# Performance work log

Measured on AMD Instinct MI355X. Metric: run time of the kernel, lower is better.

Reference implementation:

```python
import jax, jax.numpy as jnp
import numpy as np

EPS = 1e-5
KH = KW = 3  # deformable kernel
K = KH * KW


def _offset_conv(w, woff, boff):
    # standard 3x3 conv, stride 1, padding 1, NCHW
    out = jax.lax.conv_general_dilated(
        w, woff, window_strides=(1, 1), padding='SAME',
        dimension_numbers=('NCHW', 'OIHW', 'NCHW'))
    return out + boff[None, :, None, None]


def _deform_conv(feat, offset, wd, bd):
    # feat: [B,C,H,W]; offset: [B,2K,H,W] with (dy,dx) pairs per kernel point
    B, C, H, W = feat.shape
    off = offset.reshape(B, K, 2, H, W)
    ii = jnp.arange(H, dtype=feat.dtype)[:, None]  # [H,1]
    jj = jnp.arange(W, dtype=feat.dtype)[None, :]  # [1,W]
    kk = jnp.arange(K)
    ky = (kk // KW - 1).astype(feat.dtype)[None, :, None, None]  # [1,K,1,1]
    kx = (kk % KW - 1).astype(feat.dtype)[None, :, None, None]
    py = ii[None, None] + ky + off[:, :, 0]  # [B,K,H,W] sample rows
    px = jj[None, None] + kx + off[:, :, 1]  # [B,K,H,W] sample cols

    featf = feat.reshape(B, C, H * W)
    y0 = jnp.floor(py)
    x0 = jnp.floor(px)
    sampled = jnp.zeros((B, C, K, H, W), dtype=feat.dtype)
    for dy in (0, 1):
        for dx in (0, 1):
            yc = y0 + dy
            xc = x0 + dx
            wgt = (1.0 - jnp.abs(py - yc)) * (1.0 - jnp.abs(px - xc))
            valid = (yc >= 0) & (yc <= H - 1) & (xc >= 0) & (xc <= W - 1)
            wgt = jnp.where(valid, wgt, 0.0)  # zero padding outside
            yi = jnp.clip(yc, 0, H - 1).astype(jnp.int32)
            xi = jnp.clip(xc, 0, W - 1).astype(jnp.int32)
            idx = (yi * W + xi).reshape(B, 1, K * H * W)
            vals = jnp.take_along_axis(featf, idx, axis=2).reshape(B, C, K, H, W)
            sampled = sampled + vals * wgt[:, None]
    # weighted 3x3 conv over sampled points
    out = jnp.einsum('bckhw,ock->bohw', sampled, wd.reshape(wd.shape[0], C, K))
    return out + bd[None, :, None, None]


def setup_inputs() -> dict:
    key = jax.random.key(0)
    ks = jax.random.split(key, 13)
    B, Cin, H, W = 8, 256, 96, 96
    Cm = 64
    s1 = 1.0 / np.sqrt(Cin)
    s3 = 1.0 / np.sqrt(Cm * 9)
    return {
        'x': jax.random.normal(ks[0], (B, Cin, H, W), jnp.float32),
        'w1': jax.random.normal(ks[1], (Cm, Cin), jnp.float32) * s1,
        'b1': jax.random.normal(ks[2], (Cm,), jnp.float32) * s1,
        'woff': jax.random.normal(ks[3], (18, Cm, 3, 3), jnp.float32) * s3,
        'boff': jax.random.normal(ks[4], (18,), jnp.float32) * s3,
        'wd': jax.random.normal(ks[5], (Cm, Cm, 3, 3), jnp.float32) * s3,
        'bd': jax.random.normal(ks[6], (Cm,), jnp.float32) * s3,
        'gamma': jnp.ones((Cm,), jnp.float32),
        'beta': jnp.zeros((Cm,), jnp.float32),
        'rmean': jnp.zeros((Cm,), jnp.float32),
        'rvar': jax.random.uniform(ks[7], (Cm,), jnp.float32, 0.5, 1.5),
        'w2': jax.random.normal(ks[8], (Cin, Cm), jnp.float32) / np.sqrt(Cm),
        'b2': jax.random.normal(ks[9], (Cin,), jnp.float32) / np.sqrt(Cm),
    }


def reference(x, w1, b1, woff, boff, wd, bd, gamma, beta, rmean, rvar, w2, b2):
    # pwconv1 (1x1)
    w = jnp.einsum('bchw,oc->bohw', x, w1) + b1[None, :, None, None]
    # deformable 3x3 conv with predicted offsets
    off = _offset_conv(w, woff, boff)
    w = _deform_conv(w, off, wd, bd)
    # BatchNorm (eval mode, running stats)
    inv = gamma / jnp.sqrt(rvar + EPS)
    w = w * inv[None, :, None, None] + (beta - rmean * inv)[None, :, None, None]
    # pwconv2 (1x1) + sigmoid gate
    w = jnp.einsum('bchw,oc->bohw', w, w2) + b2[None, :, None, None]
    return x * jax.nn.sigmoid(w)
```

## Files before the change

kernel.cpp:

```cpp
#include <hip/hip_runtime.h>
#include <math.h>

#define H 96
#define W 96
#define HW 9216
#define B 8
#define CIN 256
#define CM 64
#define NPOS (B*HW)
#define NBLK (NPOS/64)

__device__ __forceinline__ int xswiz(int n) { return (n & 7) * 144 + (n >> 3); }

typedef float  f32x4  __attribute__((ext_vector_type(4)));
typedef short  bf16x8 __attribute__((ext_vector_type(8)));

#define OFF_WOFFT 0
#define OFF_BNS   10368
#define OFF_BNB   10432
#define OFF_WDB1  10496
#define OFF_WDB3  18688
#define OFF_WDB2  37120
#define OFF_FEAT  45312
#define OFF_FCL   4763904
#define OFF_OFFS  9482496
#define OFF_VCL   OFF_FEAT

__device__ __forceinline__ unsigned bfbits(float f) {
  union { float f; unsigned u; } c;
  c.f = f;
  return (c.u + 0x7FFFu + ((c.u >> 16) & 1u)) >> 16;
}
__device__ __forceinline__ short f2bf(float f) { return (short)bfbits(f); }
__device__ __forceinline__ unsigned pack2(float lo, float hi) {
  return bfbits(lo) | (bfbits(hi) << 16);
}

__device__ __forceinline__ bf16x8 cvt_frag(const float* p) {
  const float2* q = (const float2*)p;
  float2 a0 = q[0], a1 = q[1], a2 = q[2], a3 = q[3];
  union { unsigned u[4]; bf16x8 v; } r;
  r.u[0] = pack2(a0.x, a0.y);
  r.u[1] = pack2(a1.x, a1.y);
  r.u[2] = pack2(a2.x, a2.y);
  r.u[3] = pack2(a3.x, a3.y);
  return r.v;
}

__global__ __launch_bounds__(256) void k0_prep(
    const float* __restrict__ w1, const float* __restrict__ woff,
    const float* __restrict__ wd, const float* __restrict__ w2,
    const float* __restrict__ gamma, const float* __restrict__ beta,
    const float* __restrict__ rmean, const float* __restrict__ rvar,
    float* __restrict__ ws) {
  int i = blockIdx.x * 256 + threadIdx.x;
  if (i < 10368) {
    int c = i / 162, r = i - c * 162;
    int o = r / 9, k = r - o * 9;
    ws[OFF_WOFFT + i] = woff[(o * 64 + c) * 9 + k];
  } else if (i < 10432) {
    int o = i - 10368;
    float inv = gamma[o] / sqrtf(rvar[o] + 1e-5f);
    ws[OFF_BNS + o] = inv;
    ws[OFF_BNB + o] = beta[o] - rmean[o] * inv;
  } else if (i < 26816) {
    int j = i - 10432;
    int j8 = j & 7, lane = (j >> 3) & 63, nt = (j >> 9) & 3, kc = j >> 11;
    int n = nt * 16 + (lane & 15);
    int c = kc * 32 + ((lane >> 4) & 3) * 8 + j8;
    ((short*)(ws + OFF_WDB1))[j] = f2bf(w1[n * 256 + c]);
  } else if (i < 63680) {
    int j = i - 26816;
    int j8 = j & 7, lane = (j >> 3) & 63, nt = (j >> 9) & 3, kc = j >> 11;
    int n = nt * 16 + (lane & 15);
    int c = (kc & 1) * 32 + ((lane >> 4) & 3) * 8 + j8;
    int ks = kc >> 1;
    ((short*)(ws + OFF_WDB3))[j] = f2bf(wd[(n * 64 + c) * 9 + ks]);
  } else if (i < 80064) {
    int j = i - 63680;
    int j8 = j & 7, lane = (j >> 3) & 63, nt = (j >> 9) & 15, kc = j >> 13;
    int n = nt * 16 + (lane & 15);
    int c = kc * 32 + ((lane >> 4) & 3) * 8 + j8;
    ((short*)(ws + OFF_WDB2))[j] = f2bf(w2[n * 64 + c]);
  }
}

__global__ __launch_bounds__(256) void k1_pw1(
    const float* __restrict__ x, const short* __restrict__ wdb1,
    const float* __restrict__ b1, float* __restrict__ feat,
    float* __restrict__ fcl) {
  __shared__ float sA[64 * 66];
  int t = threadIdx.x;
  int lane = t & 63;
  int qq = __builtin_amdgcn_readfirstlane(t >> 6);
  int quad = lane >> 4, l15 = lane & 15;
  int mrow = qq * 16 + l15;
  int gpos0 = blockIdx.x * 64;
  int b = gpos0 / HW, hw0 = gpos0 - b * HW;
  f32x4 acc[4];
#pragma unroll
  for (int nt = 0; nt < 4; nt++) acc[nt] = (f32x4){0.f, 0.f, 0.f, 0.f};

  for (int c0 = 0; c0 < CIN; c0 += 64) {
#pragma unroll 4
    for (int it = 0; it < 16; it++) {
      int ci = it * 4 + quad;
      int p = qq * 16 + l15;
      sA[p * 66 + ci] = x[(size_t)(b * CIN + c0 + ci) * HW + hw0 + p];
    }
#pragma unroll
    for (int ch = 0; ch < 2; ch++) {
      bf16x8 af = cvt_frag(&sA[mrow * 66 + ch * 32 + quad * 8]);
      int kc = (c0 >> 5) + ch;
#pragma unroll
      for (int nt = 0; nt < 4; nt++) {
        bf16x8 bf = ((const bf16x8*)wdb1)[(kc * 4 + nt) * 64 + lane];
        acc[nt] = __builtin_amdgcn_mfma_f32_16x16x32_bf16(af, bf, acc[nt], 0, 0, 0);
      }
    }
  }
  __syncthreads();
#pragma unroll
  for (int nt = 0; nt < 4; nt++) {
    int o = nt * 16 + l15;
#pragma unroll
    for (int reg = 0; reg < 4; reg++) {
      int m = qq * 16 + quad * 4 + reg;
      sA[m * 66 + o] = acc[nt][reg] + b1[o];
    }
  }
  __syncthreads();
  for (int rr = t; rr < 4096; rr += 256) {
    int o1 = rr >> 6, p1 = rr & 63;
    feat[(size_t)(b * CM + o1) * HW + hw0 + p1] = sA[p1 * 66 + o1];
    int p2 = rr >> 6, o2 = rr & 63;
    fcl[(size_t)(gpos0 + p2) * 64 + o2] = sA[p2 * 66 + o2];
  }
}

__global__ __launch_bounds__(256) void k2_off(
    const float* __restrict__ feat, const float* __restrict__ wofft,
    const float* __restrict__ boff, float* __restrict__ offs) {
  __shared__ float part[4 * 18 * 64];
  int t = threadIdx.x;
  int pos = t & 63;
  int gg = __builtin_amdgcn_readfirstlane(t >> 6);
  int gpos0 = xswiz(blockIdx.x) * 64;
  int b = gpos0 / HW, hw0 = gpos0 - b * HW;
  int hw = hw0 + pos;
  int i = hw / W, j = hw - i * W;
  int idx9[9];
  float m9[9];
#pragma unroll
  for (int kh = 0; kh < 3; kh++)
#pragma unroll
    for (int kw = 0; kw < 3; kw++) {
      int yy = i + kh - 1, xx = j + kw - 1;
      bool ok = (yy >= 0) && (yy < H) && (xx >= 0) && (xx < W);
      idx9[kh * 3 + kw] = ok ? yy * W + xx : 0;
      m9[kh * 3 + kw] = ok ? 1.f : 0.f;
    }
  const float* fb = feat + (size_t)b * CM * HW;
  float acc[18];
#pragma unroll
  for (int o = 0; o < 18; o++) acc[o] = 0.f;
  for (int cc = 0; cc < 16; cc++) {
    int c = gg * 16 + cc;
    const float* fc = fb + c * HW;
    float v[9];
#pragma unroll
    for (int k = 0; k < 9; k++) v[k] = fc[idx9[k]] * m9[k];
    const float* wr = wofft + c * 162;
#pragma unroll
    for (int o = 0; o < 18; o++)
#pragma unroll
      for (int k = 0; k < 9; k++)
        acc[o] += v[k] * wr[o * 9 + k];
  }
#pragma unroll
  for (int o = 0; o < 18; o++) part[(gg * 18 + o) * 64 + pos] = acc[o];
  __syncthreads();
  for (int r = t; r < 18 * 64; r += 256) {
    int o = r >> 6, p = r & 63;
    float s = part[o * 64 + p] + part[(18 + o) * 64 + p] +
              part[(36 + o) * 64 + p] + part[(54 + o) * 64 + p] + boff[o];
    offs[(size_t)b * 18 * HW + o * HW + hw0 + p] = s;
  }
}

__global__ __launch_bounds__(256) void k3_deform(
    const float* __restrict__ fcl, const float* __restrict__ offs,
    const short* __restrict__ wdb3, const float* __restrict__ bd,
    const float* __restrict__ bns, const float* __restrict__ bnb,
    short* __restrict__ vclb) {
  __shared__ __align__(16) short sAb[64 * 72];
  __shared__ int2 tiw[4][576];
  int t = threadIdx.x;
  int lane = t & 63;
  int qq = __builtin_amdgcn_readfirstlane(t >> 6);
  int quad = lane >> 4, l15 = lane & 15;
  int mrow = qq * 16 + l15;
  int gpos0 = xswiz(blockIdx.x) * 64;
  int b = gpos0 / HW, hw0 = gpos0 - b * HW;
  int hw = hw0 + lane;
  int i = hw / W, j = hw - i * W;
  const float* ob = offs + (size_t)b * 18 * HW + hw;

  for (int k = qq; k < 9; k += 4) {
    float dy = ob[(2 * k + 0) * HW];
    float dx = ob[(2 * k + 1) * HW];
    float py = (float)(i + k / 3 - 1) + dy;
    float px = (float)(j + k % 3 - 1) + dx;
    float y0f = floorf(py), x0f = floorf(px);
    int y0 = (int)y0f, x0 = (int)x0f;
    float fy = py - y0f, fx = px - x0f;
    float w00 = (1.f - fy) * (1.f - fx), w01 = (1.f - fy) * fx;
    float w10 = fy * (1.f - fx), w11 = fy * fx;
    bool vy0 = (y0 >= 0) && (y0 < H), vy1 = (y0 + 1 >= 0) && (y0 + 1 < H);
    bool vx0 = (x0 >= 0) && (x0 < W), vx1 = (x0 + 1 >= 0) && (x0 + 1 < W);
    if (!(vy0 && vx0)) w00 = 0.f;
    if (!(vy0 && vx1)) w01 = 0.f;
    if (!(vy1 && vx0)) w10 = 0.f;
    if (!(vy1 && vx1)) w11 = 0.f;
    int yi0 = min(max(y0, 0), H - 1), yi1 = min(max(y0 + 1, 0), H - 1);
    int xi0 = min(max(x0, 0), W - 1), xi1 = min(max(x0 + 1, 0), W - 1);
    int e = k * 64 + lane;
    tiw[0][e] = make_int2((yi0 * W + xi0) * 256, __float_as_int(w00));
    tiw[1][e] = make_int2((yi0 * W + xi1) * 256, __float_as_int(w01));
    tiw[2][e] = make_int2((yi1 * W + xi0) * 256, __float_as_int(w10));
    tiw[3][e] = make_int2((yi1 * W + xi1) * 256, __float_as_int(w11));
  }
  __syncthreads();

  const char* fbase = (const char*)fcl + (size_t)b * HW * 256;
  int c2 = lane & 31;
  int c28 = c2 * 8;
  int half = lane >> 5;

  f32x4 acc[4];
#pragma unroll
  for (int nt = 0; nt < 4; nt++) acc[nt] = (f32x4){0.f, 0.f, 0.f, 0.f};

  for (int ks = 0; ks < 9; ks++) {
#pragma unroll 4
    for (int pp = 0; pp < 8; pp++) {
      int pa = qq * 16 + pp * 2 + half;
      int e = ks * 64 + pa;
      int2 t0 = tiw[0][e], t1 = tiw[1][e], t2 = tiw[2][e], t3 = tiw[3][e];
      float2 v0 = *(const float2*)(fbase + (t0.x + c28));
      float2 v1 = *(const float2*)(fbase + (t1.x + c28));
      float2 v2 = *(const float2*)(fbase + (t2.x + c28));
      float2 v3 = *(const float2*)(fbase + (t3.x + c28));
      float w0 = __int_as_float(t0.y), w1 = __int_as_float(t1.y);
      float w2 = __int_as_float(t2.y), w3 = __int_as_float(t3.y);
      float slo = w0 * v0.x + w1 * v1.x + w2 * v2.x + w3 * v3.x;
      float shi = w0 * v0.y + w1 * v1.y + w2 * v2.y + w3 * v3.y;
      ((unsigned*)sAb)[pa * 36 + c2] = pack2(slo, shi);
    }
#pragma unroll
    for (int ch = 0; ch < 2; ch++) {
      bf16x8 af = *(const bf16x8*)(sAb + mrow * 72 + ch * 32 + quad * 8);
      int kc = ks * 2 + ch;
#pragma unroll
      for (int nt = 0; nt < 4; nt++) {
        bf16x8 bf = ((const bf16x8*)wdb3)[(kc * 4 + nt) * 64 + lane];
        acc[nt] = __builtin_amdgcn_mfma_f32_16x16x32_bf16(af, bf, acc[nt], 0, 0, 0);
      }
    }
  }
  __syncthreads();
#pragma unroll
  for (int nt = 0; nt < 4; nt++) {
    int o = nt * 16 + l15;
    float sc = bns[o], sb = bnb[o], bb = bd[o];
#pragma unroll
    for (int reg = 0; reg < 4; reg++) {
      int m = qq * 16 + quad * 4 + reg;
      sAb[m * 72 + o] = f2bf((acc[nt][reg] + bb) * sc + sb);
    }
  }
  __syncthreads();
  for (int rr = t; rr < 2048; rr += 256) {
    int p = rr >> 5, cc = rr & 31;
    ((unsigned*)vclb)[(size_t)(gpos0 + p) * 32 + cc] = ((unsigned*)sAb)[p * 36 + cc];
  }
}

__global__ __launch_bounds__(256) void k4_pw2(
    const float* __restrict__ x, const short* __restrict__ vclb,
    const short* __restrict__ wdb2, const float* __restrict__ b2,
    float* __restrict__ out) {
  __shared__ float sA[64 * 66];
  int t = threadIdx.x;
  int lane = t & 63;
  int qq = __builtin_amdgcn_readfirstlane(t >> 6);
  int quad = lane >> 4, l15 = lane & 15;
  int mrow = qq * 16 + l15;
  int gpos0 = blockIdx.x * 64;
  int b = gpos0 / HW, hw0 = gpos0 - b * HW;

  const bf16x8* ap = (const bf16x8*)(vclb + (size_t)(gpos0 + mrow) * 64);
  bf16x8 af0 = ap[quad];
  bf16x8 af1 = ap[4 + quad];

  f32x4 acc[16];
#pragma unroll
  for (int nt = 0; nt < 16; nt++) acc[nt] = (f32x4){0.f, 0.f, 0.f, 0.f};
#pragma unroll
  for (int nt = 0; nt < 16; nt++) {
    bf16x8 bf0 = ((const bf16x8*)wdb2)[(0 * 16 + nt) * 64 + lane];
    bf16x8 bf1 = ((const bf16x8*)wdb2)[(1 * 16 + nt) * 64 + lane];
    acc[nt] = __builtin_amdgcn_mfma_f32_16x16x32_bf16(af0, bf0, acc[nt], 0, 0, 0);
    acc[nt] = __builtin_amdgcn_mfma_f32_16x16x32_bf16(af1, bf1, acc[nt], 0, 0, 0);
  }
  for (int nc = 0; nc < 4; nc++) {
    __syncthreads();
#pragma unroll
    for (int nt2 = 0; nt2 < 4; nt2++) {
      int nt = nc * 4 + nt2;
      int o1 = nt2 * 16 + l15;
#pragma unroll
      for (int reg = 0; reg < 4; reg++) {
        int m = qq * 16 + quad * 4 + reg;
        sA[m * 66 + o1] = acc[nt][reg] + b2[nc * 64 + nt2 * 16 + l15];
      }
    }
    __syncthreads();
    for (int rr = t; rr < 4096; rr += 256) {
      int o1 = rr >> 6, p = rr & 63;
      int o = nc * 64 + o1;
      float wv = sA[p * 66 + o1];
      float sg = 1.f / (1.f + __expf(-wv));
      size_t gi = ((size_t)b * CIN + o) * HW + hw0 + p;
      out[gi] = x[gi] * sg;
    }
  }
}

extern "C" void kernel_launch(void* const* d_in, const int* in_sizes, int n_in,
                              void* d_out, int out_size, void* d_ws, size_t ws_size,
                              hipStream_t stream) {
  const float* x     = (const float*)d_in[0];
  const float* w1    = (const float*)d_in[1];
  const float* b1    = (const float*)d_in[2];
  const float* woff  = (const float*)d_in[3];
  const float* boff  = (const float*)d_in[4];
  const float* wd    = (const float*)d_in[5];
  const float* bd    = (const float*)d_in[6];
  const float* gamma = (const float*)d_in[7];
  const float* beta  = (const float*)d_in[8];
  const float* rmean = (const float*)d_in[9];
  const float* rvar  = (const float*)d_in[10];
  const float* w2    = (const float*)d_in[11];
  const float* b2    = (const float*)d_in[12];
  float* out = (float*)d_out;
  float* ws  = (float*)d_ws;

  dim3 blk(256);
  k0_prep<<<dim3(313), blk, 0, stream>>>(w1, woff, wd, w2, gamma, beta, rmean, rvar, ws);
  k1_pw1<<<dim3(NBLK), blk, 0, stream>>>(x, (const short*)(ws + OFF_WDB1), b1,
                                         ws + OFF_FEAT, ws + OFF_FCL);
  k2_off<<<dim3(NBLK), blk, 0, stream>>>(ws + OFF_FEAT, ws + OFF_WOFFT, boff, ws + OFF_OFFS);
  k3_deform<<<dim3(NBLK), blk, 0, stream>>>(ws + OFF_FCL, ws + OFF_OFFS,
                                            (const short*)(ws + OFF_WDB3), bd,
                                            ws + OFF_BNS, ws + OFF_BNB,
                                            (short*)(ws + OFF_VCL));
  k4_pw2<<<dim3(NBLK), blk, 0, stream>>>(x, (const short*)(ws + OFF_VCL),
                                         (const short*)(ws + OFF_WDB2), b2, out);
}
```

Measured before the change: 302.6 us.

## Move offset conv to MFMA, drop NCHW feat copy, gather bilinear directly into fragments

The offset-prediction 3x3 conv now runs as a bf16 MFMA GEMM over the channels-last feature buffer instead of scalar FMAs over an NCHW copy. The NCHW feat write in pwconv1 is therefore removed. pwconv1 loads x straight into MFMA fragments without LDS staging, and the deformable kernel builds A fragments directly from float4 gathers instead of going through shared memory. It also adds block swizzling to k1 and k4, and trades some precision in the offset conv (now bf16) for less memory traffic and FMA work.

```diff
diff --git a/kernel.cpp b/kernel.cpp
--- a/kernel.cpp
+++ b/kernel.cpp
@@ -15,16 +15,15 @@
 typedef float  f32x4  __attribute__((ext_vector_type(4)));
 typedef short  bf16x8 __attribute__((ext_vector_type(8)));
 
-#define OFF_WOFFT 0
-#define OFF_BNS   10368
-#define OFF_BNB   10432
-#define OFF_WDB1  10496
-#define OFF_WDB3  18688
-#define OFF_WDB2  37120
-#define OFF_FEAT  45312
-#define OFF_FCL   4763904
-#define OFF_OFFS  9482496
-#define OFF_VCL   OFF_FEAT
+#define OFF_WDBO  0
+#define OFF_BNS   9216
+#define OFF_BNB   9280
+#define OFF_WDB1  9344
+#define OFF_WDB3  17536
+#define OFF_WDB2  35968
+#define OFF_FCL   44160
+#define OFF_OFFS  4762752
+#define OFF_VCL   6089856
 
 __device__ __forceinline__ unsigned bfbits(float f) {
   union { float f; unsigned u; } c;
@@ -34,17 +33,6 @@
 __device__ __forceinline__ short f2bf(float f) { return (short)bfbits(f); }
 __device__ __forceinline__ unsigned pack2(float lo, float hi) {
   return bfbits(lo) | (bfbits(hi) << 16);
-}
-
-__device__ __forceinline__ bf16x8 cvt_frag(const float* p) {
-  const float2* q = (const float2*)p;
-  float2 a0 = q[0], a1 = q[1], a2 = q[2], a3 = q[3];
-  union { unsigned u[4]; bf16x8 v; } r;
-  r.u[0] = pack2(a0.x, a0.y);
-  r.u[1] = pack2(a1.x, a1.y);
-  r.u[2] = pack2(a2.x, a2.y);
-  r.u[3] = pack2(a3.x, a3.y);
-  return r.v;
 }
 
 __global__ __launch_bounds__(256) void k0_prep(
@@ -54,30 +42,33 @@
     const float* __restrict__ rmean, const float* __restrict__ rvar,
     float* __restrict__ ws) {
   int i = blockIdx.x * 256 + threadIdx.x;
-  if (i < 10368) {
-    int c = i / 162, r = i - c * 162;
-    int o = r / 9, k = r - o * 9;
-    ws[OFF_WOFFT + i] = woff[(o * 64 + c) * 9 + k];
-  } else if (i < 10432) {
-    int o = i - 10368;
+  if (i < 18432) {
+    int j = i;
+    int j8 = j & 7, lane = (j >> 3) & 63, nt = (j >> 9) & 1, kc = j >> 10;
+    int n = nt * 16 + (lane & 15);
+    int c = (kc & 1) * 32 + ((lane >> 4) & 3) * 8 + j8;
+    int ks = kc >> 1;
+    ((short*)(ws + OFF_WDBO))[j] = (n < 18) ? f2bf(woff[(n * 64 + c) * 9 + ks]) : (short)0;
+  } else if (i < 18496) {
+    int o = i - 18432;
     float inv = gamma[o] / sqrtf(rvar[o] + 1e-5f);
     ws[OFF_BNS + o] = inv;
     ws[OFF_BNB + o] = beta[o] - rmean[o] * inv;
-  } else if (i < 26816) {
-    int j = i - 10432;
+  } else if (i < 34880) {
+    int j = i - 18496;
     int j8 = j & 7, lane = (j >> 3) & 63, nt = (j >> 9) & 3, kc = j >> 11;
     int n = nt * 16 + (lane & 15);
     int c = kc * 32 + ((lane >> 4) & 3) * 8 + j8;
     ((short*)(ws + OFF_WDB1))[j] = f2bf(w1[n * 256 + c]);
-  } else if (i < 63680) {
-    int j = i - 26816;
+  } else if (i < 71744) {
+    int j = i - 34880;
     int j8 = j & 7, lane = (j >> 3) & 63, nt = (j >> 9) & 3, kc = j >> 11;
     int n = nt * 16 + (lane & 15);
     int c = (kc & 1) * 32 + ((lane >> 4) & 3) * 8 + j8;
     int ks = kc >> 1;
     ((short*)(ws + OFF_WDB3))[j] = f2bf(wd[(n * 64 + c) * 9 + ks]);
-  } else if (i < 80064) {
-    int j = i - 63680;
+  } else if (i < 88128) {
+    int j = i - 71744;
     int j8 = j & 7, lane = (j >> 3) & 63, nt = (j >> 9) & 15, kc = j >> 13;
     int n = nt * 16 + (lane & 15);
     int c = kc * 32 + ((lane >> 4) & 3) * 8 + j8;
@@ -87,39 +78,33 @@
 
 __global__ __launch_bounds__(256) void k1_pw1(
     const float* __restrict__ x, const short* __restrict__ wdb1,
-    const float* __restrict__ b1, float* __restrict__ feat,
-    float* __restrict__ fcl) {
+    const float* __restrict__ b1, float* __restrict__ fcl) {
   __shared__ float sA[64 * 66];
   int t = threadIdx.x;
   int lane = t & 63;
   int qq = __builtin_amdgcn_readfirstlane(t >> 6);
   int quad = lane >> 4, l15 = lane & 15;
-  int mrow = qq * 16 + l15;
-  int gpos0 = blockIdx.x * 64;
+  int gpos0 = xswiz(blockIdx.x) * 64;
   int b = gpos0 / HW, hw0 = gpos0 - b * HW;
+  const float* xp = x + (size_t)b * CIN * HW + (size_t)(quad * 8) * HW + hw0 + qq * 16 + l15;
   f32x4 acc[4];
 #pragma unroll
   for (int nt = 0; nt < 4; nt++) acc[nt] = (f32x4){0.f, 0.f, 0.f, 0.f};
 
-  for (int c0 = 0; c0 < CIN; c0 += 64) {
-#pragma unroll 4
-    for (int it = 0; it < 16; it++) {
-      int ci = it * 4 + quad;
-      int p = qq * 16 + l15;
-      sA[p * 66 + ci] = x[(size_t)(b * CIN + c0 + ci) * HW + hw0 + p];
-    }
-#pragma unroll
-    for (int ch = 0; ch < 2; ch++) {
-      bf16x8 af = cvt_frag(&sA[mrow * 66 + ch * 32 + quad * 8]);
-      int kc = (c0 >> 5) + ch;
-#pragma unroll
-      for (int nt = 0; nt < 4; nt++) {
-        bf16x8 bf = ((const bf16x8*)wdb1)[(kc * 4 + nt) * 64 + lane];
-        acc[nt] = __builtin_amdgcn_mfma_f32_16x16x32_bf16(af, bf, acc[nt], 0, 0, 0);
-      }
-    }
-  }
-  __syncthreads();
+#pragma unroll 2
+  for (int kc = 0; kc < 8; kc++) {
+    float v[8];
+#pragma unroll
+    for (int j = 0; j < 8; j++) v[j] = xp[(size_t)(kc * 32 + j) * HW];
+    union { unsigned u[4]; bf16x8 f; } af;
+    af.u[0] = pack2(v[0], v[1]); af.u[1] = pack2(v[2], v[3]);
+    af.u[2] = pack2(v[4], v[5]); af.u[3] = pack2(v[6], v[7]);
+#pragma unroll
+    for (int nt = 0; nt < 4; nt++) {
+      bf16x8 bf = ((const bf16x8*)wdb1)[(kc * 4 + nt) * 64 + lane];
+      acc[nt] = __builtin_amdgcn_mfma_f32_16x16x32_bf16(af.f, bf, acc[nt], 0, 0, 0);
+    }
+  }
 #pragma unroll
   for (int nt = 0; nt < 4; nt++) {
     int o = nt * 16 + l15;
@@ -131,60 +116,60 @@
   }
   __syncthreads();
   for (int rr = t; rr < 4096; rr += 256) {
-    int o1 = rr >> 6, p1 = rr & 63;
-    feat[(size_t)(b * CM + o1) * HW + hw0 + p1] = sA[p1 * 66 + o1];
     int p2 = rr >> 6, o2 = rr & 63;
     fcl[(size_t)(gpos0 + p2) * 64 + o2] = sA[p2 * 66 + o2];
   }
 }
 
 __global__ __launch_bounds__(256) void k2_off(
-    const float* __restrict__ feat, const float* __restrict__ wofft,
+    const float* __restrict__ fcl, const short* __restrict__ wdbo,
     const float* __restrict__ boff, float* __restrict__ offs) {
-  __shared__ float part[4 * 18 * 64];
+  __shared__ float sP[64 * 34];
   int t = threadIdx.x;
-  int pos = t & 63;
-  int gg = __builtin_amdgcn_readfirstlane(t >> 6);
+  int lane = t & 63;
+  int qq = __builtin_amdgcn_readfirstlane(t >> 6);
+  int quad = lane >> 4, l15 = lane & 15;
   int gpos0 = xswiz(blockIdx.x) * 64;
   int b = gpos0 / HW, hw0 = gpos0 - b * HW;
-  int hw = hw0 + pos;
-  int i = hw / W, j = hw - i * W;
-  int idx9[9];
-  float m9[9];
-#pragma unroll
-  for (int kh = 0; kh < 3; kh++)
-#pragma unroll
-    for (int kw = 0; kw < 3; kw++) {
-      int yy = i + kh - 1, xx = j + kw - 1;
-      bool ok = (yy >= 0) && (yy < H) && (xx >= 0) && (xx < W);
-      idx9[kh * 3 + kw] = ok ? yy * W + xx : 0;
-      m9[kh * 3 + kw] = ok ? 1.f : 0.f;
-    }
-  const float* fb = feat + (size_t)b * CM * HW;
-  float acc[18];
-#pragma unroll
-  for (int o = 0; o < 18; o++) acc[o] = 0.f;
-  for (int cc = 0; cc < 16; cc++) {
-    int c = gg * 16 + cc;
-    const float* fc = fb + c * HW;
-    float v[9];
-#pragma unroll
-    for (int k = 0; k < 9; k++) v[k] = fc[idx9[k]] * m9[k];
-    const float* wr = wofft + c * 162;
-#pragma unroll
-    for (int o = 0; o < 18; o++)
-#pragma unroll
-      for (int k = 0; k < 9; k++)
-        acc[o] += v[k] * wr[o * 9 + k];
-  }
-#pragma unroll
-  for (int o = 0; o < 18; o++) part[(gg * 18 + o) * 64 + pos] = acc[o];
+  int m = qq * 16 + l15;
+  int hw = hw0 + m, i = hw / W, j = hw - i * W;
+  f32x4 acc[2];
+  acc[0] = (f32x4){0.f, 0.f, 0.f, 0.f};
+  acc[1] = (f32x4){0.f, 0.f, 0.f, 0.f};
+
+#pragma unroll 1
+  for (int ks = 0; ks < 9; ks++) {
+    int dy = ks / 3 - 1, dx = ks % 3 - 1;
+    bool ok = ((unsigned)(i + dy) < (unsigned)H) && ((unsigned)(j + dx) < (unsigned)W);
+    int spos = gpos0 + m + (ok ? dy * W + dx : 0);
+    const float* src = fcl + (size_t)spos * 64 + quad * 8;
+#pragma unroll
+    for (int ch = 0; ch < 2; ch++) {
+      f32x4 va = *(const f32x4*)(src + ch * 32);
+      f32x4 vb = *(const f32x4*)(src + ch * 32 + 4);
+      if (!ok) { va = (f32x4){0.f,0.f,0.f,0.f}; vb = (f32x4){0.f,0.f,0.f,0.f}; }
+      union { unsigned u[4]; bf16x8 f; } af;
+      af.u[0] = pack2(va[0], va[1]); af.u[1] = pack2(va[2], va[3]);
+      af.u[2] = pack2(vb[0], vb[1]); af.u[3] = pack2(vb[2], vb[3]);
+      int kc = ks * 2 + ch;
+#pragma unroll
+      for (int nt = 0; nt < 2; nt++) {
+        bf16x8 bf = ((const bf16x8*)wdbo)[(kc * 2 + nt) * 64 + lane];
+        acc[nt] = __builtin_amdgcn_mfma_f32_16x16x32_bf16(af.f, bf, acc[nt], 0, 0, 0);
+      }
+    }
+  }
+#pragma unroll
+  for (int nt = 0; nt < 2; nt++)
+#pragma unroll
+    for (int reg = 0; reg < 4; reg++) {
+      int mm = qq * 16 + quad * 4 + reg;
+      sP[mm * 34 + nt * 16 + l15] = acc[nt][reg];
+    }
   __syncthreads();
-  for (int r = t; r < 18 * 64; r += 256) {
-    int o = r >> 6, p = r & 63;
-    float s = part[o * 64 + p] + part[(18 + o) * 64 + p] +
-              part[(36 + o) * 64 + p] + part[(54 + o) * 64 + p] + boff[o];
-    offs[(size_t)b * 18 * HW + o * HW + hw0 + p] = s;
+  for (int rr = t; rr < 18 * 64; rr += 256) {
+    int o = rr >> 6, p = rr & 63;
+    offs[((size_t)b * 18 + o) * HW + hw0 + p] = sP[p * 34 + o] + boff[o];
   }
 }
 
@@ -193,8 +178,8 @@
     const short* __restrict__ wdb3, const float* __restrict__ bd,
     const float* __restrict__ bns, const float* __restrict__ bnb,
     short* __restrict__ vclb) {
-  __shared__ __align__(16) short sAb[64 * 72];
   __shared__ int2 tiw[4][576];
+  __shared__ __align__(16) short sEp[64 * 72];
   int t = threadIdx.x;
   int lane = t & 63;
   int qq = __builtin_amdgcn_readfirstlane(t >> 6);
@@ -232,43 +217,41 @@
   }
   __syncthreads();
 
-  const char* fbase = (const char*)fcl + (size_t)b * HW * 256;
-  int c2 = lane & 31;
-  int c28 = c2 * 8;
-  int half = lane >> 5;
-
+  const char* fb = (const char*)fcl + (size_t)b * HW * 256;
   f32x4 acc[4];
 #pragma unroll
   for (int nt = 0; nt < 4; nt++) acc[nt] = (f32x4){0.f, 0.f, 0.f, 0.f};
 
+#pragma unroll 1
   for (int ks = 0; ks < 9; ks++) {
-#pragma unroll 4
-    for (int pp = 0; pp < 8; pp++) {
-      int pa = qq * 16 + pp * 2 + half;
-      int e = ks * 64 + pa;
-      int2 t0 = tiw[0][e], t1 = tiw[1][e], t2 = tiw[2][e], t3 = tiw[3][e];
-      float2 v0 = *(const float2*)(fbase + (t0.x + c28));
-      float2 v1 = *(const float2*)(fbase + (t1.x + c28));
-      float2 v2 = *(const float2*)(fbase + (t2.x + c28));
-      float2 v3 = *(const float2*)(fbase + (t3.x + c28));
-      float w0 = __int_as_float(t0.y), w1 = __int_as_float(t1.y);
-      float w2 = __int_as_float(t2.y), w3 = __int_as_float(t3.y);
-      float slo = w0 * v0.x + w1 * v1.x + w2 * v2.x + w3 * v3.x;
-      float shi = w0 * v0.y + w1 * v1.y + w2 * v2.y + w3 * v3.y;
-      ((unsigned*)sAb)[pa * 36 + c2] = pack2(slo, shi);
-    }
+    int e = ks * 64 + mrow;
+    int2 t0 = tiw[0][e], t1 = tiw[1][e], t2 = tiw[2][e], t3 = tiw[3][e];
+    float w0 = __int_as_float(t0.y), w1 = __int_as_float(t1.y);
+    float w2 = __int_as_float(t2.y), w3 = __int_as_float(t3.y);
 #pragma unroll
     for (int ch = 0; ch < 2; ch++) {
-      bf16x8 af = *(const bf16x8*)(sAb + mrow * 72 + ch * 32 + quad * 8);
+      int bo = ch * 128 + quad * 32;
+      f32x4 va0 = *(const f32x4*)(fb + (t0.x + bo));
+      f32x4 va1 = *(const f32x4*)(fb + (t1.x + bo));
+      f32x4 va2 = *(const f32x4*)(fb + (t2.x + bo));
+      f32x4 va3 = *(const f32x4*)(fb + (t3.x + bo));
+      f32x4 vb0 = *(const f32x4*)(fb + (t0.x + bo + 16));
+      f32x4 vb1 = *(const f32x4*)(fb + (t1.x + bo + 16));
+      f32x4 vb2 = *(const f32x4*)(fb + (t2.x + bo + 16));
+      f32x4 vb3 = *(const f32x4*)(fb + (t3.x + bo + 16));
+      f32x4 slo = w0 * va0 + w1 * va1 + w2 * va2 + w3 * va3;
+      f32x4 shi = w0 * vb0 + w1 * vb1 + w2 * vb2 + w3 * vb3;
+      union { unsigned u[4]; bf16x8 f; } af;
+      af.u[0] = pack2(slo[0], slo[1]); af.u[1] = pack2(slo[2], slo[3]);
+      af.u[2] = pack2(shi[0], shi[1]); af.u[3] = pack2(shi[2], shi[3]);
       int kc = ks * 2 + ch;
 #pragma unroll
       for (int nt = 0; nt < 4; nt++) {
         bf16x8 bf = ((const bf16x8*)wdb3)[(kc * 4 + nt) * 64 + lane];
-        acc[nt] = __builtin_amdgcn_mfma_f32_16x16x32_bf16(af, bf, acc[nt], 0, 0, 0);
+        acc[nt] = __builtin_amdgcn_mfma_f32_16x16x32_bf16(af.f, bf, acc[nt], 0, 0, 0);
       }
     }
   }
-  __syncthreads();
 #pragma unroll
   for (int nt = 0; nt < 4; nt++) {
     int o = nt * 16 + l15;
@@ -276,13 +259,13 @@
 #pragma unroll
     for (int reg = 0; reg < 4; reg++) {
       int m = qq * 16 + quad * 4 + reg;
-      sAb[m * 72 + o] = f2bf((acc[nt][reg] + bb) * sc + sb);
+      sEp[m * 72 + o] = f2bf((acc[nt][reg] + bb) * sc + sb);
     }
   }
   __syncthreads();
   for (int rr = t; rr < 2048; rr += 256) {
     int p = rr >> 5, cc = rr & 31;
-    ((unsigned*)vclb)[(size_t)(gpos0 + p) * 32 + cc] = ((unsigned*)sAb)[p * 36 + cc];
+    ((unsigned*)vclb)[(size_t)(gpos0 + p) * 32 + cc] = ((const unsigned*)sEp)[p * 36 + cc];
   }
 }
 
@@ -296,7 +279,7 @@
   int qq = __builtin_amdgcn_readfirstlane(t >> 6);
   int quad = lane >> 4, l15 = lane & 15;
   int mrow = qq * 16 + l15;
-  int gpos0 = blockIdx.x * 64;
+  int gpos0 = xswiz(blockIdx.x) * 64;
   int b = gpos0 / HW, hw0 = gpos0 - b * HW;
 
   const bf16x8* ap = (const bf16x8*)(vclb + (size_t)(gpos0 + mrow) * 64);
@@ -357,10 +340,10 @@
   float* ws  = (float*)d_ws;
 
   dim3 blk(256);
-  k0_prep<<<dim3(313), blk, 0, stream>>>(w1, woff, wd, w2, gamma, beta, rmean, rvar, ws);
-  k1_pw1<<<dim3(NBLK), blk, 0, stream>>>(x, (const short*)(ws + OFF_WDB1), b1,
-                                         ws + OFF_FEAT, ws + OFF_FCL);
-  k2_off<<<dim3(NBLK), blk, 0, stream>>>(ws + OFF_FEAT, ws + OFF_WOFFT, boff, ws + OFF_OFFS);
+  k0_prep<<<dim3(345), blk, 0, stream>>>(w1, woff, wd, w2, gamma, beta, rmean, rvar, ws);
+  k1_pw1<<<dim3(NBLK), blk, 0, stream>>>(x, (const short*)(ws + OFF_WDB1), b1, ws + OFF_FCL);
+  k2_off<<<dim3(NBLK), blk, 0, stream>>>(ws + OFF_FCL, (const short*)(ws + OFF_WDBO),
+                                         boff, ws + OFF_OFFS);
   k3_deform<<<dim3(NBLK), blk, 0, stream>>>(ws + OFF_FCL, ws + OFF_OFFS,
                                             (const short*)(ws + OFF_WDB3), bd,
                                             ws + OFF_BNS, ws + OFF_BNB,
```

Result: slower. 324.2 us (+7.1%).
